# Kernel optimization log

Measured on AMD Instinct MI355X. Metric: run time of the kernel, lower is better.

The kernel has to match this reference:

```python
import jax, jax.numpy as jnp
import numpy as np

D_MODEL = 512
KERNEL = 16
DILATIONS = (1, 1, 2, 2, 4, 4, 8, 8)
HEADS = len(DILATIONS)
HEAD_W = D_MODEL // HEADS
B, L = 2, 1024
MODE = "forward"  # causal: window sees only prior words


def setup_inputs() -> dict:
    key = jax.random.key(0)
    ks = jax.random.split(key, 8)
    s = 0.02  # small init like nn.Linear
    return {
        "tensor": jax.random.normal(ks[0], (B, L, D_MODEL), jnp.float32),
        "Wq": jax.random.normal(ks[1], (HEADS, HEAD_W, D_MODEL), jnp.float32) * s,
        "bq": jnp.zeros((HEADS, HEAD_W), jnp.float32),
        "Wk": jax.random.normal(ks[2], (HEADS, KERNEL, HEAD_W, D_MODEL), jnp.float32) * s,
        "bk": jnp.zeros((HEADS, KERNEL, HEAD_W), jnp.float32),
        "Wv": jax.random.normal(ks[3], (HEADS, KERNEL, HEAD_W, D_MODEL), jnp.float32) * s,
        "bv": jnp.zeros((HEADS, KERNEL, HEAD_W), jnp.float32),
        "Wo": jax.random.normal(ks[4], (D_MODEL, HEADS, HEAD_W), jnp.float32) * s,
        "bo": jnp.zeros((D_MODEL,), jnp.float32),
    }


def _window_indices():
    """Static gather indices replicating Glimpses.dilocal's dilated unfold.

    Returns idx of shape (H, L, K) indexing into a sequence zero-padded by
    max_off on both sides: content[h, l, k] = x_padded[idx[h, l, k]].
    """
    dil = np.asarray(DILATIONS)  # (H,)
    max_off = int((KERNEL - 1) * dil.max())
    if MODE == "forward":
        front = (KERNEL - 1) * dil           # all padding in front (causal)
    elif MODE == "backward":
        front = np.zeros_like(dil)           # all padding behind
    else:  # center
        front = ((KERNEL - 1) * dil) // 2
    l = np.arange(L)[None, :, None]
    k = np.arange(KERNEL)[None, None, :]
    d = dil[:, None, None]
    f = front[:, None, None]
    idx = l + k * d - f + max_off            # (H, L, K), always in-range
    return jnp.asarray(idx), max_off


_IDX, _MOFF = _window_indices()


def reference(tensor, Wq, bq, Wk, bk, Wv, bv, Wo, bo):
    # tensor: (B, L, D)
    xp = jnp.pad(tensor, ((0, 0), (_MOFF, _MOFF), (0, 0)))
    content = xp[:, _IDX, :]                                   # (B,H,L,K,D)
    # per-head query projection (kernel position 1)
    q = jnp.einsum('bld,hod->bhlo', tensor, Wq) + bq[:, None, :]        # (B,H,L,hw)
    # per-(head, kernel-position) independent key/value projections
    k = jnp.einsum('bhlkd,hkod->bhlko', content, Wk) + bk[:, None, :, :]
    v = jnp.einsum('bhlkd,hkod->bhlko', content, Wv) + bv[:, None, :, :]
    # tiny local attention over the K window positions
    logits = jnp.einsum('bhlo,bhlko->bhlk', q, k)               # (B,H,L,K)
    score = jax.nn.softmax(logits, axis=-1)
    # NOTE: original scales AFTER the score@value matmul (faithful to source)
    attn = jnp.einsum('bhlk,bhlko->bhlo', score, v)
    attn = attn / jnp.sqrt(jnp.asarray(HEAD_W, tensor.dtype))   # (B,H,L,hw)
    # dehead: merge (heads, head_width) -> d_model
    out = jnp.einsum('bhlo,dho->bld', attn, Wo) + bo            # (B,L,D)
    return out
```

## Files before the change

kernel.cpp:

```cpp
#include <hip/hip_runtime.h>


#define BD 2
#define LL 1024
#define DM 512
#define HH 8
#define KT 16
#define HW 64

#define NQKV 16896

typedef unsigned short u16;
typedef unsigned int u32;
typedef __bf16 bf16x8 __attribute__((ext_vector_type(8)));
typedef float f32x4 __attribute__((ext_vector_type(4)));
typedef unsigned short ushort4v __attribute__((ext_vector_type(4)));
typedef unsigned short ushort8v __attribute__((ext_vector_type(8)));

__constant__ int c_dil[8] = {1, 1, 2, 2, 4, 4, 8, 8};

__device__ __forceinline__ float bf2f(u16 u) {
    return __builtin_bit_cast(float, (u32)u << 16);
}
__device__ __forceinline__ u16 f2bf(float f) {
    u32 u = __builtin_bit_cast(u32, f);
    return (u16)((u + 0x7fffu + ((u >> 16) & 1u)) >> 16);
}

__device__ __forceinline__ void gl_lds16(const u16* g, u16* l) {
    __builtin_amdgcn_global_load_lds(
        (__attribute__((address_space(1))) void*)g,
        (__attribute__((address_space(3))) void*)l, 16, 0, 0);
}

__global__ __launch_bounds__(256, 4) void gemm_bf16(
    const u16* __restrict__ A, const u16* __restrict__ Bm,
    const float* __restrict__ bq, const float* __restrict__ bk,
    const float* __restrict__ bv, u16* __restrict__ C)
{
    const int m0 = blockIdx.y << 7;
    const int n0 = blockIdx.x << 7;
    if (n0 >= NQKV) return;

    __shared__ u16 As[128 * 32];
    __shared__ u16 Bs[128 * 32];

    const int tid  = threadIdx.x;
    const int wave = tid >> 6, lane = tid & 63;
    const int r0 = tid >> 2;
    const int cc = (tid & 3) << 3;
    const int mw = (wave >> 1) << 6;
    const int nw = (wave & 1) << 6;
    const int lr = lane & 15;
    const int qg = lane >> 4;
    const int ksw = ((qg ^ ((lr >> 1) & 3)) << 3);

    const u16* Ag = A  + (size_t)(m0 + r0) * DM + cc;
    const u16* Bg = Bm + (size_t)(n0 + r0) * DM + cc;
    u16* lA = &As[0] + tid * 8;
    u16* lB = &Bs[0] + tid * 8;

    f32x4 acc[4][4];
#pragma unroll
    for (int i = 0; i < 4; ++i)
#pragma unroll
        for (int j = 0; j < 4; ++j) acc[i][j] = (f32x4){0.f, 0.f, 0.f, 0.f};

    for (int k0 = 0; k0 < DM; k0 += 32) {
        gl_lds16(Ag + k0, lA);
        gl_lds16(Ag + k0 + (size_t)64 * DM, lA + 64 * 32);
        gl_lds16(Bg + k0, lB);
        gl_lds16(Bg + k0 + (size_t)64 * DM, lB + 64 * 32);
        __syncthreads();

        bf16x8 af[4], bfr[4];
#pragma unroll
        for (int i = 0; i < 4; ++i)
            af[i] = *(const bf16x8*)&As[(mw + (i << 4) + lr) * 32 + ksw];
#pragma unroll
        for (int j = 0; j < 4; ++j)
            bfr[j] = *(const bf16x8*)&Bs[(nw + (j << 4) + lr) * 32 + ksw];
#pragma unroll
        for (int i = 0; i < 4; ++i)
#pragma unroll
            for (int j = 0; j < 4; ++j)
                acc[i][j] = __builtin_amdgcn_mfma_f32_16x16x32_bf16(
                    af[i], bfr[j], acc[i][j], 0, 0, 0);
        __syncthreads();
    }

    const float* bias; int cb;
    if      (n0 <  512) { bias = bq; cb = 0;    }
    else if (n0 < 8704) { bias = bk; cb = 512;  }
    else                { bias = bv; cb = 8704; }

#pragma unroll
    for (int i = 0; i < 4; ++i) {
        const int rowb = m0 + mw + (i << 4) + (qg << 2);
#pragma unroll
        for (int j = 0; j < 4; ++j) {
            const int col = n0 + nw + (j << 4) + lr;
            const float bs = bias[col - cb];
#pragma unroll
            for (int r = 0; r < 4; ++r)
                __builtin_nontemporal_store(
                    f2bf(acc[i][j][r] + bs),
                    &C[(size_t)(rowb + r) * NQKV + col]);
        }
    }
}

__global__ __launch_bounds__(256, 4) void gemm_out(
    const u16* __restrict__ A, const u16* __restrict__ Bm,
    const float* __restrict__ bias, float* __restrict__ C)
{
    __shared__ u16 As[64 * 32];
    __shared__ u16 Bs[64 * 32];

    const int tid  = threadIdx.x;
    const int wave = tid >> 6, lane = tid & 63;
    const int m0 = blockIdx.y << 6, n0 = blockIdx.x << 6;
    const int r0 = tid >> 2, cc = (tid & 3) << 3;
    const int mw = wave << 4;
    const int lr = lane & 15, qg = lane >> 4;
    const int ksw = ((qg ^ ((lr >> 1) & 3)) << 3);

    const u16* Ag = A  + (size_t)(m0 + r0) * DM + cc;
    const u16* Bg = Bm + (size_t)(n0 + r0) * DM + cc;
    u16* lA = &As[0] + tid * 8;
    u16* lB = &Bs[0] + tid * 8;

    f32x4 acc[4];
#pragma unroll
    for (int j = 0; j < 4; ++j) acc[j] = (f32x4){0.f, 0.f, 0.f, 0.f};

    for (int k0 = 0; k0 < DM; k0 += 32) {
        gl_lds16(Ag + k0, lA);
        gl_lds16(Bg + k0, lB);
        __syncthreads();
        bf16x8 af = *(const bf16x8*)&As[(mw + lr) * 32 + ksw];
#pragma unroll
        for (int j = 0; j < 4; ++j) {
            bf16x8 bfr = *(const bf16x8*)&Bs[((j << 4) + lr) * 32 + ksw];
            acc[j] = __builtin_amdgcn_mfma_f32_16x16x32_bf16(af, bfr, acc[j], 0, 0, 0);
        }
        __syncthreads();
    }

#pragma unroll
    for (int j = 0; j < 4; ++j) {
        const int col = n0 + (j << 4) + lr;
        const float bs = bias[col];
#pragma unroll
        for (int r = 0; r < 4; ++r)
            C[(size_t)(m0 + mw + (qg << 2) + r) * DM + col] = acc[j][r] + bs;
    }
}

__global__ void cvt_swz(const float* __restrict__ x,  const float* __restrict__ Wq,
                        const float* __restrict__ Wk, const float* __restrict__ Wv,
                        const float* __restrict__ Wo,
                        u16* __restrict__ xb, u16* __restrict__ wb,
                        u16* __restrict__ wob)
{
    const int i = blockIdx.x * 256 + threadIdx.x;
    const float* src; u16* dst; int t;
    if (i < 131072) {
        t = i;
        src = x;  dst = xb;
    } else if (i < 1212416) {
        t = i - 131072;
        const int row = t >> 6;
        if      (row <  512) src = Wq;
        else if (row < 8704) src = Wk - (size_t)512 * DM;
        else                 src = Wv - (size_t)8704 * DM;
        dst = wb;
    } else {
        t = i - 1212416;
        src = Wo; dst = wob;
    }
    const int row = t >> 6;
    const int c8  = t & 63;
    const int s   = (row >> 1) & 3;
    const int oc  = (c8 & ~3) | ((c8 & 3) ^ s);
    const float* p = src + (size_t)row * DM + (oc << 3);
    float4 v0 = *(const float4*)p;
    float4 v1 = *(const float4*)(p + 4);
    ushort8v o = { f2bf(v0.x), f2bf(v0.y), f2bf(v0.z), f2bf(v0.w),
                   f2bf(v1.x), f2bf(v1.y), f2bf(v1.z), f2bf(v1.w) };
    *(ushort8v*)(dst + (size_t)row * DM + (c8 << 3)) = o;
}

__global__ __launch_bounds__(256, 4) void attn_bf16(
    const u16* __restrict__ qkv,
    const float* __restrict__ bk,
    const float* __restrict__ bv,
    u16* __restrict__ attnb)
{
    const int tid = threadIdx.x;
    const int j  = tid & 7;
    const int ll = tid >> 3;
    const int bid = blockIdx.x;
    const int h = bid & 7;
    const int t = (bid >> 3) & 31;
    const int b = bid >> 8;
    const int l = (t << 5) + ll;
    const int dil = c_dil[h];

    const int hko = h * (KT * HW);
    const size_t rowbase = (size_t)(b * LL) * NQKV + hko + (j << 3);

    float qf[8];
    {
        ushort8v qv = __builtin_nontemporal_load(
            (const ushort8v*)(qkv + (size_t)(b * LL + l) * NQKV + h * HW + (j << 3)));
#pragma unroll
        for (int z = 0; z < 8; ++z) qf[z] = bf2f(qv[z]);
    }

    ushort8v kr[KT];
#pragma unroll
    for (int k = 0; k < KT; ++k) {
        const int src = l - (KT - 1 - k) * dil;
        if (src >= 0)
            kr[k] = __builtin_nontemporal_load(
                (const ushort8v*)(qkv + rowbase + (size_t)src * NQKV + 512 + k * HW));
    }

    float lg[KT];
#pragma unroll
    for (int k = 0; k < KT; ++k) {
        const int src = l - (KT - 1 - k) * dil;
        float p = 0.f;
        if (src >= 0) {
#pragma unroll
            for (int z = 0; z < 8; ++z) p += qf[z] * bf2f(kr[k][z]);
        } else {
            const float* bkp = bk + hko + k * HW + (j << 3);
#pragma unroll
            for (int z = 0; z < 8; ++z) p += qf[z] * bkp[z];
        }
        p += __shfl_xor(p, 1);
        p += __shfl_xor(p, 2);
        p += __shfl_xor(p, 4);
        lg[k] = p;
    }

    float m = lg[0];
#pragma unroll
    for (int k = 1; k < KT; ++k) m = fmaxf(m, lg[k]);
    float s = 0.f;
#pragma unroll
    for (int k = 0; k < KT; ++k) { lg[k] = __expf(lg[k] - m); s += lg[k]; }
    const float inv = 1.f / s;

    ushort8v vr[KT];
#pragma unroll
    for (int k = 0; k < KT; ++k) {
        const int src = l - (KT - 1 - k) * dil;
        if (src >= 0)
            vr[k] = __builtin_nontemporal_load(
                (const ushort8v*)(qkv + rowbase + (size_t)src * NQKV + 8704 + k * HW));
    }

    float acc[8];
#pragma unroll
    for (int z = 0; z < 8; ++z) acc[z] = 0.f;
#pragma unroll
    for (int k = 0; k < KT; ++k) {
        const int src = l - (KT - 1 - k) * dil;
        const float sc = lg[k] * inv;
        if (src >= 0) {
#pragma unroll
            for (int z = 0; z < 8; ++z) acc[z] = fmaf(sc, bf2f(vr[k][z]), acc[z]);
        } else {
            const float* bvp = bv + hko + k * HW + (j << 3);
#pragma unroll
            for (int z = 0; z < 8; ++z) acc[z] = fmaf(sc, bvp[z], acc[z]);
        }
    }

    ushort8v o;
#pragma unroll
    for (int z = 0; z < 8; ++z) o[z] = f2bf(acc[z] * 0.125f);
    const int row = b * LL + l;
    const int k8 = h * 8 + j;
    const int sw = ((k8 & 3) ^ ((l >> 1) & 3)) << 3;
    *(ushort8v*)(attnb + (size_t)row * DM + ((k8 >> 2) << 5) + sw) = o;
}

__global__ __launch_bounds__(256, 2) void gemm_nt_bias(
    const float* __restrict__ A, const float* __restrict__ Bm,
    const float* __restrict__ bias, float* __restrict__ C,
    int M, int N, int Kd)
{
    __shared__ float As[16][68];
    __shared__ float Bs[16][68];
    const int tid = threadIdx.x;
    const int tx = tid & 15, ty = tid >> 4;
    const int r0 = blockIdx.y << 6, c0 = blockIdx.x << 6;
    const int lr = tid >> 2, k4 = (tid & 3) << 2;
    const float* Ap = A  + (size_t)(r0 + lr) * Kd + k4;
    const float* Bp = Bm + (size_t)(c0 + lr) * Kd + k4;
    float acc[4][4];
#pragma unroll
    for (int i = 0; i < 4; ++i)
#pragma unroll
        for (int j = 0; j < 4; ++j) acc[i][j] = 0.f;
    for (int d0 = 0; d0 < Kd; d0 += 16) {
        float4 av = *(const float4*)(Ap + d0);
        float4 bv = *(const float4*)(Bp + d0);
        As[k4 + 0][lr] = av.x; As[k4 + 1][lr] = av.y;
        As[k4 + 2][lr] = av.z; As[k4 + 3][lr] = av.w;
        Bs[k4 + 0][lr] = bv.x; Bs[k4 + 1][lr] = bv.y;
        Bs[k4 + 2][lr] = bv.z; Bs[k4 + 3][lr] = bv.w;
        __syncthreads();
#pragma unroll
        for (int dd = 0; dd < 16; ++dd) {
            float4 a4 = *(const float4*)&As[dd][ty << 2];
            float4 b4 = *(const float4*)&Bs[dd][tx << 2];
            float ar[4] = {a4.x, a4.y, a4.z, a4.w};
            float br[4] = {b4.x, b4.y, b4.z, b4.w};
#pragma unroll
            for (int i = 0; i < 4; ++i)
#pragma unroll
                for (int j = 0; j < 4; ++j)
                    acc[i][j] = fmaf(ar[i], br[j], acc[i][j]);
        }
        __syncthreads();
    }
#pragma unroll
    for (int i = 0; i < 4; ++i) {
        float4 o;
        const int c = c0 + (tx << 2);
        o.x = acc[i][0] + bias[c + 0];
        o.y = acc[i][1] + bias[c + 1];
        o.z = acc[i][2] + bias[c + 2];
        o.w = acc[i][3] + bias[c + 3];
        *(float4*)&C[(size_t)(r0 + (ty << 2) + i) * N + c] = o;
    }
}

__device__ __forceinline__ void tile_gemm_f32(
    const float* __restrict__ xb, int src, bool ok,
    const float* __restrict__ wrow,
    int lr, int k4, int tx, int ty,
    float (&As)[16][68], float (&Ws)[16][68], float (&acc)[4][4])
{
#pragma unroll
    for (int i = 0; i < 4; ++i)
#pragma unroll
        for (int j = 0; j < 4; ++j) acc[i][j] = 0.f;
    const float* xrow = xb + (size_t)(ok ? src : 0) * DM + k4;
    for (int d0 = 0; d0 < DM; d0 += 16) {
        float4 av = make_float4(0.f, 0.f, 0.f, 0.f);
        if (ok) av = *(const float4*)(xrow + d0);
        float4 wv = *(const float4*)(wrow + d0);
        As[k4 + 0][lr] = av.x; As[k4 + 1][lr] = av.y;
        As[k4 + 2][lr] = av.z; As[k4 + 3][lr] = av.w;
        Ws[k4 + 0][lr] = wv.x; Ws[k4 + 1][lr] = wv.y;
        Ws[k4 + 2][lr] = wv.z; Ws[k4 + 3][lr] = wv.w;
        __syncthreads();
#pragma unroll
        for (int dd = 0; dd < 16; ++dd) {
            float4 a4 = *(const float4*)&As[dd][ty << 2];
            float4 b4 = *(const float4*)&Ws[dd][tx << 2];
            float ar[4] = {a4.x, a4.y, a4.z, a4.w};
            float br[4] = {b4.x, b4.y, b4.z, b4.w};
#pragma unroll
            for (int i = 0; i < 4; ++i)
#pragma unroll
                for (int j = 0; j < 4; ++j)
                    acc[i][j] = fmaf(ar[i], br[j], acc[i][j]);
        }
        __syncthreads();
    }
}

__global__ __launch_bounds__(256, 2) void attn_kernel(
    const float* __restrict__ x, const float* __restrict__ q,
    const float* __restrict__ Wk, const float* __restrict__ bk,
    const float* __restrict__ Wv, const float* __restrict__ bv,
    float* __restrict__ attn)
{
    __shared__ float As[16][68];
    __shared__ float Ws[16][68];
    __shared__ float qs[64][68];
    __shared__ float lg[64][17];
    __shared__ float red[64][17];
    const int tid = threadIdx.x;
    const int tx = tid & 15, ty = tid >> 4;
    const int bid = blockIdx.x;
    const int h = bid & 7, t = (bid >> 3) & 15, b = bid >> 7;
    const int l0 = t << 6;
    const int dil = c_dil[h];
    const int lr = tid >> 2, k4 = (tid & 3) << 2;
    for (int i = tid; i < 64 * 16; i += 256) {
        int l = i >> 4, o4 = (i & 15) << 2;
        float4 v = *(const float4*)&q[((size_t)(b * LL + l0 + l) * HH + h) * HW + o4];
        *(float4*)&qs[l][o4] = v;
    }
    const float* xb  = x  + (size_t)b * LL * DM;
    const float* Wkh = Wk + (size_t)h * KT * HW * DM;
    const float* Wvh = Wv + (size_t)h * KT * HW * DM;
    const float* bkh = bk + h * KT * HW;
    const float* bvh = bv + h * KT * HW;
    float acc[4][4];
    for (int kk = 0; kk < KT; ++kk) {
        const int src = l0 + lr - (KT - 1 - kk) * dil;
        const bool ok = (src >= 0) && (src < LL);
        tile_gemm_f32(xb, src, ok, Wkh + (size_t)(kk * HW + lr) * DM + k4,
                      lr, k4, tx, ty, As, Ws, acc);
        const float* bkp = bkh + kk * HW + (tx << 2);
#pragma unroll
        for (int i = 0; i < 4; ++i) {
            float p = 0.f;
#pragma unroll
            for (int j = 0; j < 4; ++j)
                p += (acc[i][j] + bkp[j]) * qs[(ty << 2) + i][(tx << 2) + j];
            red[(ty << 2) + i][tx] = p;
        }
        __syncthreads();
        if (tid < 64) {
            float s = 0.f;
#pragma unroll
            for (int u = 0; u < 16; ++u) s += red[tid][u];
            lg[tid][kk] = s;
        }
        __syncthreads();
    }
    if (tid < 64) {
        float m = lg[tid][0];
#pragma unroll
        for (int u = 1; u < KT; ++u) m = fmaxf(m, lg[tid][u]);
        float s = 0.f;
#pragma unroll
        for (int u = 0; u < KT; ++u) {
            float e = expf(lg[tid][u] - m);
            lg[tid][u] = e; s += e;
        }
        float inv = 1.f / s;
#pragma unroll
        for (int u = 0; u < KT; ++u) lg[tid][u] *= inv;
    }
    __syncthreads();
    float vacc[4][4];
#pragma unroll
    for (int i = 0; i < 4; ++i)
#pragma unroll
        for (int j = 0; j < 4; ++j) vacc[i][j] = 0.f;
    for (int kk = 0; kk < KT; ++kk) {
        const int src = l0 + lr - (KT - 1 - kk) * dil;
        const bool ok = (src >= 0) && (src < LL);
        tile_gemm_f32(xb, src, ok, Wvh + (size_t)(kk * HW + lr) * DM + k4,
                      lr, k4, tx, ty, As, Ws, acc);
        const float* bvp = bvh + kk * HW + (tx << 2);
#pragma unroll
        for (int i = 0; i < 4; ++i) {
            float sc = lg[(ty << 2) + i][kk];
#pragma unroll
            for (int j = 0; j < 4; ++j)
                vacc[i][j] = fmaf(sc, acc[i][j] + bvp[j], vacc[i][j]);
        }
    }
#pragma unroll
    for (int i = 0; i < 4; ++i) {
        float4 o;
        o.x = vacc[i][0] * 0.125f;
        o.y = vacc[i][1] * 0.125f;
        o.z = vacc[i][2] * 0.125f;
        o.w = vacc[i][3] * 0.125f;
        *(float4*)&attn[((size_t)(b * LL + l0 + (ty << 2) + i) * HH + h) * HW + (tx << 2)] = o;
    }
}

extern "C" void kernel_launch(void* const* d_in, const int* in_sizes, int n_in,
                              void* d_out, int out_size, void* d_ws, size_t ws_size,
                              hipStream_t stream)
{
    const float* x  = (const float*)d_in[0];
    const float* Wq = (const float*)d_in[1];
    const float* bq = (const float*)d_in[2];
    const float* Wk = (const float*)d_in[3];
    const float* bk = (const float*)d_in[4];
    const float* Wv = (const float*)d_in[5];
    const float* bv = (const float*)d_in[6];
    const float* Wo = (const float*)d_in[7];
    const float* bo = (const float*)d_in[8];
    float* out = (float*)d_out;

    const int M = BD * LL;

    const size_t N_X   = (size_t)BD * LL * DM;
    const size_t N_WB  = (size_t)NQKV * DM;
    const size_t N_WO  = (size_t)DM * DM;
    const size_t N_QKV = (size_t)M * NQKV;
    const size_t NEED  = (N_X + N_WB + N_WO + N_QKV + N_X) * 2;

    if (ws_size >= NEED) {
        u16* xb    = (u16*)d_ws;
        u16* wb    = xb    + N_X;
        u16* wob   = wb    + N_WB;
        u16* qkv   = wob   + N_WO;
        u16* attnb = qkv   + N_QKV;

        cvt_swz<<<4864, 256, 0, stream>>>(x, Wq, Wk, Wv, Wo, xb, wb, wob);

        gemm_bf16<<<dim3(136, 16), 256, 0, stream>>>(
            xb, wb, bq, bk, bv, qkv);

        attn_bf16<<<BD * HH * (LL / 32), 256, 0, stream>>>(
            qkv, bk, bv, attnb);

        gemm_out<<<dim3(8, 32), 256, 0, stream>>>(attnb, wob, bo, out);
    } else {
        float* qws = (float*)d_ws;
        float* aws = qws + (size_t)BD * LL * HH * HW;
        gemm_nt_bias<<<dim3((HH * HW) / 64, M / 64), 256, 0, stream>>>(
            x, Wq, bq, qws, M, HH * HW, DM);
        attn_kernel<<<BD * HH * (LL / 64), 256, 0, stream>>>(
            x, qws, Wk, bk, Wv, bv, aws);
        gemm_nt_bias<<<dim3(DM / 64, M / 64), 256, 0, stream>>>(
            aws, Wo, bo, out, M, DM, HH * HW);
    }
}
```

Measured before the change: 180.0 us.

## Fuse local attention with output projection into single kernel

Result: faster. 173.3 us (-3.7%).

```diff
diff --git a/kernel.cpp b/kernel.cpp
--- a/kernel.cpp
+++ b/kernel.cpp
@@ -103,57 +103,8 @@
             const float bs = bias[col - cb];
 #pragma unroll
             for (int r = 0; r < 4; ++r)
-                __builtin_nontemporal_store(
-                    f2bf(acc[i][j][r] + bs),
-                    &C[(size_t)(rowb + r) * NQKV + col]);
-        }
-    }
-}
-
-__global__ __launch_bounds__(256, 4) void gemm_out(
-    const u16* __restrict__ A, const u16* __restrict__ Bm,
-    const float* __restrict__ bias, float* __restrict__ C)
-{
-    __shared__ u16 As[64 * 32];
-    __shared__ u16 Bs[64 * 32];
-
-    const int tid  = threadIdx.x;
-    const int wave = tid >> 6, lane = tid & 63;
-    const int m0 = blockIdx.y << 6, n0 = blockIdx.x << 6;
-    const int r0 = tid >> 2, cc = (tid & 3) << 3;
-    const int mw = wave << 4;
-    const int lr = lane & 15, qg = lane >> 4;
-    const int ksw = ((qg ^ ((lr >> 1) & 3)) << 3);
-
-    const u16* Ag = A  + (size_t)(m0 + r0) * DM + cc;
-    const u16* Bg = Bm + (size_t)(n0 + r0) * DM + cc;
-    u16* lA = &As[0] + tid * 8;
-    u16* lB = &Bs[0] + tid * 8;
-
-    f32x4 acc[4];
-#pragma unroll
-    for (int j = 0; j < 4; ++j) acc[j] = (f32x4){0.f, 0.f, 0.f, 0.f};
-
-    for (int k0 = 0; k0 < DM; k0 += 32) {
-        gl_lds16(Ag + k0, lA);
-        gl_lds16(Bg + k0, lB);
-        __syncthreads();
-        bf16x8 af = *(const bf16x8*)&As[(mw + lr) * 32 + ksw];
-#pragma unroll
-        for (int j = 0; j < 4; ++j) {
-            bf16x8 bfr = *(const bf16x8*)&Bs[((j << 4) + lr) * 32 + ksw];
-            acc[j] = __builtin_amdgcn_mfma_f32_16x16x32_bf16(af, bfr, acc[j], 0, 0, 0);
-        }
-        __syncthreads();
-    }
-
-#pragma unroll
-    for (int j = 0; j < 4; ++j) {
-        const int col = n0 + (j << 4) + lr;
-        const float bs = bias[col];
-#pragma unroll
-        for (int r = 0; r < 4; ++r)
-            C[(size_t)(m0 + mw + (qg << 2) + r) * DM + col] = acc[j][r] + bs;
+                C[(size_t)(rowb + r) * NQKV + col] = f2bf(acc[i][j][r] + bs);
+        }
     }
 }
 
@@ -164,7 +115,7 @@
                         u16* __restrict__ wob)
 {
     const int i = blockIdx.x * 256 + threadIdx.x;
-    const float* src; u16* dst; int t;
+    const float* src; u16* dst; int t; bool swz = true;
     if (i < 131072) {
         t = i;
         src = x;  dst = xb;
@@ -177,11 +128,11 @@
         dst = wb;
     } else {
         t = i - 1212416;
-        src = Wo; dst = wob;
+        src = Wo; dst = wob; swz = false;
     }
     const int row = t >> 6;
     const int c8  = t & 63;
-    const int s   = (row >> 1) & 3;
+    const int s   = swz ? ((row >> 1) & 3) : 0;
     const int oc  = (c8 & ~3) | ((c8 & 3) ^ s);
     const float* p = src + (size_t)row * DM + (oc << 3);
     float4 v0 = *(const float4*)p;
@@ -191,20 +142,23 @@
     *(ushort8v*)(dst + (size_t)row * DM + (c8 << 3)) = o;
 }
 
-__global__ __launch_bounds__(256, 4) void attn_bf16(
+__global__ __launch_bounds__(512, 2) void attn_out(
     const u16* __restrict__ qkv,
     const float* __restrict__ bk,
     const float* __restrict__ bv,
-    u16* __restrict__ attnb)
-{
+    const u16* __restrict__ wob,
+    const float* __restrict__ bo,
+    float* __restrict__ out)
+{
+    __shared__ u16 at[16 * 512];
+
     const int tid = threadIdx.x;
     const int j  = tid & 7;
-    const int ll = tid >> 3;
+    const int h  = (tid >> 3) & 7;
+    const int li = tid >> 6;
     const int bid = blockIdx.x;
-    const int h = bid & 7;
-    const int t = (bid >> 3) & 31;
-    const int b = bid >> 8;
-    const int l = (t << 5) + ll;
+    const int b = bid >> 7;
+    const int l = ((bid & 127) << 3) + li;
     const int dil = c_dil[h];
 
     const int hko = h * (KT * HW);
@@ -280,13 +234,48 @@
         }
     }
 
-    ushort8v o;
-#pragma unroll
-    for (int z = 0; z < 8; ++z) o[z] = f2bf(acc[z] * 0.125f);
-    const int row = b * LL + l;
-    const int k8 = h * 8 + j;
-    const int sw = ((k8 & 3) ^ ((l >> 1) & 3)) << 3;
-    *(ushort8v*)(attnb + (size_t)row * DM + ((k8 >> 2) << 5) + sw) = o;
+    {
+        ushort8v o;
+#pragma unroll
+        for (int z = 0; z < 8; ++z) o[z] = f2bf(acc[z] * 0.125f);
+        const int lane = (h << 3) + j;
+        const int sc8 = (lane & ~3) | ((lane & 3) ^ ((li >> 1) & 3));
+        *(ushort8v*)&at[li * 512 + (sc8 << 3)] = o;
+    }
+
+    __syncthreads();
+
+    const int lane = tid & 63;
+    const int lr16 = lane & 15;
+    const int q4   = lane >> 4;
+    const int nw   = li << 6;
+    const int ksw  = ((q4 ^ ((lr16 >> 1) & 3)) << 3);
+
+    f32x4 oacc[4];
+#pragma unroll
+    for (int jt = 0; jt < 4; ++jt) oacc[jt] = (f32x4){0.f, 0.f, 0.f, 0.f};
+
+    for (int k0 = 0; k0 < DM; k0 += 32) {
+        bf16x8 af = *(const bf16x8*)&at[lr16 * 512 + k0 + ksw];
+#pragma unroll
+        for (int jt = 0; jt < 4; ++jt) {
+            const int col = nw + (jt << 4) + lr16;
+            bf16x8 bfr = *(const bf16x8*)(wob + (size_t)col * DM + k0 + (q4 << 3));
+            oacc[jt] = __builtin_amdgcn_mfma_f32_16x16x32_bf16(af, bfr, oacc[jt], 0, 0, 0);
+        }
+    }
+
+    if (q4 < 2) {
+        const int rowg = (bid << 3) + (q4 << 2);
+#pragma unroll
+        for (int jt = 0; jt < 4; ++jt) {
+            const int col = nw + (jt << 4) + lr16;
+            const float bs = bo[col];
+#pragma unroll
+            for (int r = 0; r < 4; ++r)
+                out[(size_t)(rowg + r) * DM + col] = oacc[jt][r] + bs;
+        }
+    }
 }
 
 __global__ __launch_bounds__(256, 2) void gemm_nt_bias(
@@ -502,17 +491,13 @@
         u16* wb    = xb    + N_X;
         u16* wob   = wb    + N_WB;
         u16* qkv   = wob   + N_WO;
-        u16* attnb = qkv   + N_QKV;
 
         cvt_swz<<<4864, 256, 0, stream>>>(x, Wq, Wk, Wv, Wo, xb, wb, wob);
 
         gemm_bf16<<<dim3(136, 16), 256, 0, stream>>>(
             xb, wb, bq, bk, bv, qkv);
 
-        attn_bf16<<<BD * HH * (LL / 32), 256, 0, stream>>>(
-            qkv, bk, bv, attnb);
-
-        gemm_out<<<dim3(8, 32), 256, 0, stream>>>(attnb, wob, bo, out);
+        attn_out<<<256, 512, 0, stream>>>(qkv, bk, bv, wob, bo, out);
     } else {
         float* qws = (float*)d_ws;
         float* aws = qws + (size_t)BD * LL * HH * HW;
```
